# Optimization experiments

Measured on AMD Instinct MI355X. Metric: run time of the kernel, lower is better.

Reference implementation:

```python
import jax, jax.numpy as jnp
import numpy as np

EMBED = 768
HEADS = 12
HEAD_DIM = EMBED // HEADS
STREAMS = 4
SK_ITERS = 20
MLP_HIDDEN = 3072
EPS_SK = 1e-8
EPS_LN = 1e-5


def setup_inputs() -> dict:
    key = jax.random.key(0)
    ks = jax.random.split(key, 16)
    w = lambda k, shape: (jax.random.normal(k, shape, dtype=jnp.float32) * 0.02)
    return {
        "x": jax.random.normal(ks[0], (8, 1024, EMBED), dtype=jnp.float32),
        "ln1_g": jnp.ones((EMBED,), jnp.float32),
        "ln1_b": jnp.zeros((EMBED,), jnp.float32),
        "ln2_g": jnp.ones((EMBED,), jnp.float32),
        "ln2_b": jnp.zeros((EMBED,), jnp.float32),
        "qkv_w": w(ks[1], (3 * EMBED, EMBED)),
        "qkv_b": jnp.zeros((3 * EMBED,), jnp.float32),
        "proj_w": w(ks[2], (EMBED, EMBED)),
        "proj_b": jnp.zeros((EMBED,), jnp.float32),
        "fc1_w": w(ks[3], (MLP_HIDDEN, EMBED)),
        "fc1_b": jnp.zeros((MLP_HIDDEN,), jnp.float32),
        "fc2_w": w(ks[4], (EMBED, MLP_HIDDEN)),
        "fc2_b": jnp.zeros((EMBED,), jnp.float32),
        "a_hres": w(ks[5], (STREAMS, STREAMS)),
        "a_hpre": w(ks[6], (STREAMS,)),
        "a_hpost": w(ks[7], (STREAMS,)),
        "m_hres": w(ks[8], (STREAMS, STREAMS)),
        "m_hpre": w(ks[9], (STREAMS,)),
        "m_hpost": w(ks[10], (STREAMS,)),
    }


def layernorm(x, g, b):
    mu = x.mean(-1, keepdims=True)
    var = ((x - mu) ** 2).mean(-1, keepdims=True)
    return (x - mu) * jax.lax.rsqrt(var + EPS_LN) * g + b


def sinkhorn_knopp(logits):
    # logits: (n, n) -> doubly-stochastic (n, n); batch expansion in torch is redundant
    A = jnp.exp(logits)
    for _ in range(SK_ITERS):
        A = A / (A.sum(-1, keepdims=True) + EPS_SK)
        A = A / (A.sum(-2, keepdims=True) + EPS_SK)
    return A


def attention(x, qkv_w, qkv_b, proj_w, proj_b):
    B, N, D = x.shape
    qkv = x @ qkv_w.T + qkv_b                      # (B, N, 3D)
    qkv = qkv.reshape(B, N, 3, HEADS, HEAD_DIM)
    q, k, v = jnp.moveaxis(qkv, 2, 0)              # each (B, N, H, hd)
    scale = HEAD_DIM ** -0.5
    scores = jnp.einsum('bqhd,bkhd->bhqk', q, k) * scale
    attn = jax.nn.softmax(scores, axis=-1)
    out = jnp.einsum('bhqk,bkhd->bqhd', attn, v).reshape(B, N, D)
    return out @ proj_w.T + proj_b


def mlp(x, fc1_w, fc1_b, fc2_w, fc2_b):
    h = jax.nn.gelu(x @ fc1_w.T + fc1_b, approximate=False)
    return h @ fc2_w.T + fc2_b


def mhc(x, hres_logits, hpre_logits, hpost_logits, transform_fn):
    B, L, D = x.shape
    n, c = STREAMS, D // STREAMS
    xs = x.reshape(B, L, n, c)
    H_res = sinkhorn_knopp(hres_logits)            # (n, n)
    H_pre = jax.nn.softmax(hpre_logits)            # (n,)
    H_post = jax.nn.softmax(hpost_logits)          # (n,)
    x_pre = jnp.einsum('n,blnc->blc', H_pre, xs)   # weighted sum over streams
    x_pre_full = jnp.tile(x_pre, (1, 1, n))        # (B, L, D)
    t = transform_fn(x_pre_full)
    t_mean = t.reshape(B, L, n, c).mean(axis=2)    # (B, L, c)
    out = (jnp.einsum('nm,blmc->blnc', H_res, xs)
           + H_post[None, None, :, None] * t_mean[:, :, None, :])
    return out.reshape(B, L, D)


def reference(x, ln1_g, ln1_b, ln2_g, ln2_b, qkv_w, qkv_b, proj_w, proj_b,
              fc1_w, fc1_b, fc2_w, fc2_b,
              a_hres, a_hpre, a_hpost, m_hres, m_hpre, m_hpost):
    x = mhc(x, a_hres, a_hpre, a_hpost,
            lambda h: attention(layernorm(h, ln1_g, ln1_b), qkv_w, qkv_b, proj_w, proj_b))
    x = mhc(x, m_hres, m_hpre, m_hpost,
            lambda h: mlp(layernorm(h, ln2_g, ln2_b), fc1_w, fc1_b, fc2_w, fc2_b))
    return x
```

## Files before the change

kernel.cpp:

```cpp
#include <hip/hip_runtime.h>
#include <hip/hip_bf16.h>
#include <cstdint>
#include <cstddef>

#define EMBED 768
#define STREAMS 4
#define CHUNK 192
#define HEADS 12
#define HD 64
#define SEQ 1024
#define BATCH 8
#define TOKENS (BATCH * SEQ)
#define MLPH 3072

typedef __bf16 bf16;
typedef __bf16 bf16x4 __attribute__((ext_vector_type(4)));
typedef __bf16 bf16x8 __attribute__((ext_vector_type(8)));
typedef float f32x4 __attribute__((ext_vector_type(4)));

#define GLDS16(gp, lp)                                                        \
  __builtin_amdgcn_global_load_lds(                                           \
      (const __attribute__((address_space(1))) void*)(gp),                    \
      (__attribute__((address_space(3))) void*)(lp), 16, 0, 0)

#define BARRIER() do { asm volatile("" ::: "memory");                         \
  __builtin_amdgcn_s_barrier(); asm volatile("" ::: "memory"); } while (0)

__global__ void hprep_kernel(const float* ar, const float* ap, const float* ao,
                             const float* mr, const float* mp, const float* mo,
                             float* HS) {
  if (threadIdx.x != 0) return;
  const float* L[2] = {ar, mr};
  const float* P[2] = {ap, mp};
  const float* O[2] = {ao, mo};
  for (int s = 0; s < 2; ++s) {
    float A[16];
    for (int i = 0; i < 16; ++i) A[i] = expf(L[s][i]);
    for (int it = 0; it < 20; ++it) {
      for (int r = 0; r < 4; ++r) {
        float rs = A[4*r] + A[4*r+1] + A[4*r+2] + A[4*r+3] + 1e-8f;
        for (int c = 0; c < 4; ++c) A[4*r+c] /= rs;
      }
      for (int c = 0; c < 4; ++c) {
        float cs = A[c] + A[4+c] + A[8+c] + A[12+c] + 1e-8f;
        for (int r = 0; r < 4; ++r) A[4*r+c] /= cs;
      }
    }
    float* dst = HS + s * 24;
    for (int i = 0; i < 16; ++i) dst[i] = A[i];
    {
      float m = fmaxf(fmaxf(P[s][0], P[s][1]), fmaxf(P[s][2], P[s][3]));
      float e[4], t = 0.f;
      for (int i = 0; i < 4; ++i) { e[i] = expf(P[s][i] - m); t += e[i]; }
      for (int i = 0; i < 4; ++i) dst[16 + i] = e[i] / t;
    }
    {
      float m = fmaxf(fmaxf(O[s][0], O[s][1]), fmaxf(O[s][2], O[s][3]));
      float e[4], t = 0.f;
      for (int i = 0; i < 4; ++i) { e[i] = expf(O[s][i] - m); t += e[i]; }
      for (int i = 0; i < 4; ++i) dst[20 + i] = e[i] / t;
    }
  }
}

__global__ void cvt_kernel(const float* __restrict__ in, bf16* __restrict__ out, int n4) {
  int i = blockIdx.x * 256 + threadIdx.x;
  const int st = gridDim.x * 256;
  for (; i < n4; i += st) {
    const float4 v = ((const float4*)in)[i];
    bf16x4 o = {(bf16)v.x, (bf16)v.y, (bf16)v.z, (bf16)v.w};
    *(bf16x4*)(out + (size_t)i * 4) = o;
  }
}

__global__ __launch_bounds__(256) void preln_kernel(
    const float* __restrict__ x, const float* __restrict__ H,
    const float* __restrict__ g, const float* __restrict__ b,
    bf16* __restrict__ out) {
  const int t = blockIdx.x;
  const float* xr = x + (size_t)t * EMBED;
  __shared__ float s[CHUNK];
  __shared__ float part[8];
  __shared__ float red[2];
  const int tid = threadIdx.x;
  float sv = 0.f;
  if (tid < CHUNK) {
    sv = H[0]*xr[tid] + H[1]*xr[CHUNK+tid] + H[2]*xr[2*CHUNK+tid] + H[3]*xr[3*CHUNK+tid];
    s[tid] = sv;
  }
  float sum = sv, sq = sv * sv;
  #pragma unroll
  for (int m = 32; m > 0; m >>= 1) {
    sum += __shfl_down(sum, m);
    sq  += __shfl_down(sq, m);
  }
  if ((tid & 63) == 0) { part[tid >> 6] = sum; part[4 + (tid >> 6)] = sq; }
  __syncthreads();
  if (tid == 0) {
    float S = part[0] + part[1] + part[2] + part[3];
    float Q = part[4] + part[5] + part[6] + part[7];
    float mu = S * (1.f / CHUNK);
    float var = Q * (1.f / CHUNK) - mu * mu;
    red[0] = mu;
    red[1] = rsqrtf(var + 1e-5f);
  }
  __syncthreads();
  const float mu = red[0], rs = red[1];
  bf16* orow = out + (size_t)t * EMBED;
  #pragma unroll
  for (int r = 0; r < 3; ++r) {
    const int d = tid + r * 256;
    const float v = (s[d % CHUNK] - mu) * rs * g[d] + b[d];
    orow[d] = (bf16)v;
  }
}

template <int GELU, int OUTF32>
__global__ __launch_bounds__(256) void gemm_bt(
    const bf16* __restrict__ A, const bf16* __restrict__ B,
    const float* __restrict__ bias, void* __restrict__ Cout,
    int M, int N, int K) {
  constexpr int BM = 128, BN = 128, BK = 32;
  __shared__ bf16 sA[2][BM * BK];
  __shared__ bf16 sB[2][BN * BK];
  const int tid  = threadIdx.x;
  const int lane = tid & 63;
  const int nwg = gridDim.x * gridDim.y;
  int Lw = blockIdx.y * gridDim.x + blockIdx.x;
  Lw = (Lw & 7) * (nwg >> 3) + (Lw >> 3);
  const int bm = (Lw / gridDim.x) * BM;
  const int bn = (Lw % gridDim.x) * BN;
  const int wave = tid >> 6;
  const int wr = (wave >> 1) * 64;
  const int wc = (wave & 1) * 64;
  f32x4 acc[4][4] = {};
  const int tr = tid >> 2;
  const int tc = (tid & 3) * 8;
  const bf16* Ag = A + (size_t)(bm + tr) * K + tc;
  const bf16* Bg = B + (size_t)(bn + tr) * K + tc;
  const int lofs = tr * BK + tc;
  const int arow = wr + (lane & 15);
  const int brow = wc + (lane & 15);
  const int k0 = (lane >> 4) * 8;
  const int nst = K / BK;
  GLDS16(Ag, sA[0] + lofs);
  GLDS16(Ag + (size_t)64 * K, sA[0] + lofs + 64 * BK);
  GLDS16(Bg, sB[0] + lofs);
  GLDS16(Bg + (size_t)64 * K, sB[0] + lofs + 64 * BK);
  for (int t = 0; t < nst; ++t) {
    const int cur = t & 1;
    if (t + 1 < nst) {
      const int bk = (t + 1) * BK;
      GLDS16(Ag + bk, sA[cur ^ 1] + lofs);
      GLDS16(Ag + (size_t)64 * K + bk, sA[cur ^ 1] + lofs + 64 * BK);
      GLDS16(Bg + bk, sB[cur ^ 1] + lofs);
      GLDS16(Bg + (size_t)64 * K + bk, sB[cur ^ 1] + lofs + 64 * BK);
      asm volatile("s_waitcnt vmcnt(4)" ::: "memory");
    } else {
      asm volatile("s_waitcnt vmcnt(0)" ::: "memory");
    }
    BARRIER();
    bf16x8 af[4], bfr[4];
    #pragma unroll
    for (int i = 0; i < 4; ++i) af[i] = *(const bf16x8*)(sA[cur] + (arow + i * 16) * BK + k0);
    #pragma unroll
    for (int j = 0; j < 4; ++j) bfr[j] = *(const bf16x8*)(sB[cur] + (brow + j * 16) * BK + k0);
    #pragma unroll
    for (int i = 0; i < 4; ++i)
      #pragma unroll
      for (int j = 0; j < 4; ++j)
        acc[i][j] = __builtin_amdgcn_mfma_f32_16x16x32_bf16(af[i], bfr[j], acc[i][j], 0, 0, 0);
    BARRIER();
  }
  const int row0 = bm + wr + ((lane >> 4) * 4);
  const int col0 = bn + wc + (lane & 15);
  #pragma unroll
  for (int j = 0; j < 4; ++j) {
    const int col = col0 + j * 16;
    const float bv = bias[col];
    #pragma unroll
    for (int i = 0; i < 4; ++i) {
      #pragma unroll
      for (int r = 0; r < 4; ++r) {
        float v = acc[i][j][r] + bv;
        if (GELU) v = 0.5f * v * (1.f + erff(v * 0.70710678118654752f));
        const size_t off = (size_t)(row0 + i * 16 + r) * N + col;
        if (OUTF32) ((float*)Cout)[off] = v;
        else        ((bf16*)Cout)[off] = (bf16)v;
      }
    }
  }
}

__global__ __launch_bounds__(256) void vt_kernel(const bf16* __restrict__ qkv,
                                                 bf16* __restrict__ VT) {
  const int tt = blockIdx.x;
  const int bh = blockIdx.y;
  const int bb = bh / HEADS;
  const int h = bh - bb * HEADS;
  __shared__ bf16 sT[64 * 64];
  const int t = threadIdx.x;
  const int srow = t >> 3;
  const int g = t & 7;
  const int gs = ((g ^ (srow & 7)) * 8);
  const bf16* Vg = qkv + ((size_t)(bb * SEQ + tt * 64 + srow)) * 2304 + 1536 + h * 64;
  GLDS16(Vg + gs, sT + srow * 64 + g * 8);
  GLDS16(Vg + (size_t)32 * 2304 + gs, sT + (32 + srow) * 64 + g * 8);
  __syncthreads();
  const int hd = t >> 2;
  const int tg = (t & 3) * 16;
  bf16 tmp[16];
  #pragma unroll
  for (int j = 0; j < 16; ++j) {
    const int tok = tg + j;
    tmp[j] = sT[tok * 64 + (hd ^ ((tok & 7) << 3))];
  }
  bf16* op = VT + (size_t)bh * (HD * SEQ) + (size_t)hd * SEQ + tt * 64 + tg;
  *(bf16x8*)(op) = *(const bf16x8*)(tmp);
  *(bf16x8*)(op + 8) = *(const bf16x8*)(tmp + 8);
}

__global__ __launch_bounds__(256) void attn_kernel(
    const bf16* __restrict__ qkv, const bf16* __restrict__ VT,
    bf16* __restrict__ out) {
  const int qt = blockIdx.x;
  const int bh = blockIdx.y;
  const int bb = bh / HEADS;
  const int h = bh - bb * HEADS;
  const int tid = threadIdx.x;
  const int lane = tid & 63;
  const int wave = tid >> 6;
  const size_t tokBase = (size_t)bb * SEQ;
  const int q0 = qt * 64;

  __shared__ bf16 sQ[64 * 64];
  __shared__ bf16 sK[2][64 * 64];
  __shared__ bf16 sV[2][80 * 64];
  __shared__ bf16 sP[4][16 * 64];

  for (int idx = tid; idx < 16 * 64; idx += 256) {
    const bf16 v = (idx < 64) ? (bf16)1.f : (bf16)0.f;
    sV[0][64 * 64 + idx] = v;
    sV[1][64 * 64 + idx] = v;
  }

  const int srow = tid >> 3;
  const int g = tid & 7;
  const int gs = ((g ^ (srow & 7)) * 8);
  {
    const bf16* Qg = qkv + (tokBase + q0 + srow) * 2304 + h * 64;
    GLDS16(Qg + gs, sQ + srow * 64 + g * 8);
    GLDS16(Qg + (size_t)32 * 2304 + gs, sQ + (32 + srow) * 64 + g * 8);
  }
  __syncthreads();
  const int l15 = lane & 15, hi = lane >> 4;
  const int ksw = (l15 & 7) << 3;
  bf16x8 qf[2];
  {
    const int qrow = wave * 16 + l15;
    const int qsw = (qrow & 7) << 3;
    #pragma unroll
    for (int ks = 0; ks < 2; ++ks)
      qf[ks] = *(const bf16x8*)(sQ + qrow * 64 + ((hi * 8 + ks * 32) ^ qsw));
  }

  f32x4 o[5] = {};
  float mrun[4];
  #pragma unroll
  for (int r = 0; r < 4; ++r) mrun[r] = -1e30f;

  const bf16* Kbase = qkv + tokBase * 2304 + 768 + h * 64;
  const bf16* Vbase = VT + (size_t)bh * (HD * SEQ);

  {
    const bf16* Kg = Kbase + (size_t)srow * 2304;
    GLDS16(Kg + gs, sK[0] + srow * 64 + g * 8);
    GLDS16(Kg + (size_t)32 * 2304 + gs, sK[0] + (32 + srow) * 64 + g * 8);
    const bf16* Vg = Vbase + (size_t)srow * SEQ;
    GLDS16(Vg + gs, sV[0] + srow * 64 + g * 8);
    GLDS16(Vg + (size_t)32 * SEQ + gs, sV[0] + (32 + srow) * 64 + g * 8);
  }

  for (int it = 0; it < SEQ / 64; ++it) {
    const int cur = it & 1;
    if (it + 1 < SEQ / 64) {
      const int kb = (it + 1) * 64;
      const bf16* Kg = Kbase + (size_t)(kb + srow) * 2304;
      GLDS16(Kg + gs, sK[cur ^ 1] + srow * 64 + g * 8);
      GLDS16(Kg + (size_t)32 * 2304 + gs, sK[cur ^ 1] + (32 + srow) * 64 + g * 8);
      const bf16* Vg = Vbase + (size_t)srow * SEQ + kb;
      GLDS16(Vg + gs, sV[cur ^ 1] + srow * 64 + g * 8);
      GLDS16(Vg + (size_t)32 * SEQ + gs, sV[cur ^ 1] + (32 + srow) * 64 + g * 8);
      asm volatile("s_waitcnt vmcnt(4)" ::: "memory");
    } else {
      asm volatile("s_waitcnt vmcnt(0)" ::: "memory");
    }
    BARRIER();
    f32x4 s[4];
    #pragma unroll
    for (int nj = 0; nj < 4; ++nj) {
      s[nj] = (f32x4){0.f, 0.f, 0.f, 0.f};
      #pragma unroll
      for (int ks = 0; ks < 2; ++ks) {
        bf16x8 kf = *(const bf16x8*)(sK[cur] + (nj * 16 + l15) * 64 + ((hi * 8 + ks * 32) ^ ksw));
        s[nj] = __builtin_amdgcn_mfma_f32_16x16x32_bf16(qf[ks], kf, s[nj], 0, 0, 0);
      }
    }
    float p[4][4], tmax[4];
    #pragma unroll
    for (int r = 0; r < 4; ++r) {
      float m = fmaxf(fmaxf(s[0][r], s[1][r]), fmaxf(s[2][r], s[3][r]));
      tmax[r] = m * 0.125f;
    }
    #pragma unroll
    for (int r = 0; r < 4; ++r) {
      #pragma unroll
      for (int mm = 1; mm < 16; mm <<= 1) tmax[r] = fmaxf(tmax[r], __shfl_xor(tmax[r], mm));
    }
    float alpha[4];
    #pragma unroll
    for (int r = 0; r < 4; ++r) {
      const float mnew = fmaxf(mrun[r], tmax[r]);
      alpha[r] = __expf(mrun[r] - mnew);
      mrun[r] = mnew;
      #pragma unroll
      for (int nj = 0; nj < 4; ++nj)
        p[nj][r] = __expf(s[nj][r] * 0.125f - mnew);
    }
    #pragma unroll
    for (int nj = 0; nj < 5; ++nj)
      #pragma unroll
      for (int r = 0; r < 4; ++r)
        o[nj][r] *= alpha[r];
    bf16* Pw = sP[wave];
    #pragma unroll
    for (int r = 0; r < 4; ++r) {
      const int prow = hi * 4 + r;
      const int psw = (prow & 7) << 3;
      #pragma unroll
      for (int nj = 0; nj < 4; ++nj)
        Pw[prow * 64 + ((nj * 16 + l15) ^ psw)] = (bf16)p[nj][r];
    }
    #pragma unroll
    for (int ks = 0; ks < 2; ++ks) {
      bf16x8 pa = *(const bf16x8*)(Pw + l15 * 64 + ((hi * 8 + ks * 32) ^ ksw));
      #pragma unroll
      for (int nj = 0; nj < 5; ++nj) {
        bf16x8 vb = *(const bf16x8*)(sV[cur] + (nj * 16 + l15) * 64 + ((hi * 8 + ks * 32) ^ ksw));
        o[nj] = __builtin_amdgcn_mfma_f32_16x16x32_bf16(pa, vb, o[nj], 0, 0, 0);
      }
    }
    BARRIER();
  }
  #pragma unroll
  for (int r = 0; r < 4; ++r) {
    const float lsum = __shfl(o[4][r], hi << 4, 64);
    const float inv = 1.f / lsum;
    const size_t row = tokBase + q0 + wave * 16 + hi * 4 + r;
    bf16* orow = out + row * EMBED + h * 64;
    #pragma unroll
    for (int nj = 0; nj < 4; ++nj)
      orow[nj * 16 + l15] = (bf16)(o[nj][r] * inv);
  }
}

__global__ void combine_kernel(const float* __restrict__ xs, const float* __restrict__ t,
                               const float* __restrict__ Hres, const float* __restrict__ Hpost,
                               float* __restrict__ outp) {
  const int idx = blockIdx.x * 256 + threadIdx.x;
  if (idx >= TOKENS * CHUNK) return;
  const int tok = idx / CHUNK;
  const int c = idx - tok * CHUNK;
  const float* xr = xs + (size_t)tok * EMBED + c;
  const float* tr = t + (size_t)tok * EMBED + c;
  const float x0 = xr[0], x1 = xr[CHUNK], x2 = xr[2 * CHUNK], x3 = xr[3 * CHUNK];
  const float tm = 0.25f * (tr[0] + tr[CHUNK] + tr[2 * CHUNK] + tr[3 * CHUNK]);
  #pragma unroll
  for (int n = 0; n < 4; ++n) {
    const float v = Hres[4*n+0]*x0 + Hres[4*n+1]*x1 + Hres[4*n+2]*x2 + Hres[4*n+3]*x3
                  + Hpost[n] * tm;
    outp[(size_t)tok * EMBED + n * CHUNK + c] = v;
  }
}

extern "C" void kernel_launch(void* const* d_in, const int* in_sizes, int n_in,
                              void* d_out, int out_size, void* d_ws, size_t ws_size,
                              hipStream_t stream) {
  const float* x       = (const float*)d_in[0];
  const float* ln1_g   = (const float*)d_in[1];
  const float* ln1_b   = (const float*)d_in[2];
  const float* ln2_g   = (const float*)d_in[3];
  const float* ln2_b   = (const float*)d_in[4];
  const float* qkv_w   = (const float*)d_in[5];
  const float* qkv_b   = (const float*)d_in[6];
  const float* proj_w  = (const float*)d_in[7];
  const float* proj_b  = (const float*)d_in[8];
  const float* fc1_w   = (const float*)d_in[9];
  const float* fc1_b   = (const float*)d_in[10];
  const float* fc2_w   = (const float*)d_in[11];
  const float* fc2_b   = (const float*)d_in[12];
  const float* a_hres  = (const float*)d_in[13];
  const float* a_hpre  = (const float*)d_in[14];
  const float* a_hpost = (const float*)d_in[15];
  const float* m_hres  = (const float*)d_in[16];
  const float* m_hpre  = (const float*)d_in[17];
  const float* m_hpost = (const float*)d_in[18];

  char* ws = (char*)d_ws;
  float* HS = (float*)(ws);
  bf16* Wq  = (bf16*)(ws + 1024);
  bf16* Wp  = (bf16*)(ws + 1024 + 3538944);
  bf16* W1  = (bf16*)(ws + 1024 + 3538944 + 1179648);
  bf16* W2  = (bf16*)(ws + 1024 + 3538944 + 1179648 + 4718592);
  bf16* LN  = (bf16*)(ws + 14156800);
  float* T  = (float*)(ws + 26739712);
  float* X2 = (float*)(ws + 51905536);
  bf16* QKV = (bf16*)(ws + 77071360);
  bf16* AO  = (bf16*)(ws + 114820096);
  bf16* Hm  = (bf16*)(ws + 77071360);
  bf16* VT  = LN;

  hprep_kernel<<<1, 64, 0, stream>>>(a_hres, a_hpre, a_hpost, m_hres, m_hpre, m_hpost, HS);
  cvt_kernel<<<1024, 256, 0, stream>>>(qkv_w, Wq, 2304 * 768 / 4);
  cvt_kernel<<<1024, 256, 0, stream>>>(proj_w, Wp, 768 * 768 / 4);
  cvt_kernel<<<1024, 256, 0, stream>>>(fc1_w, W1, 3072 * 768 / 4);
  cvt_kernel<<<1024, 256, 0, stream>>>(fc2_w, W2, 768 * 3072 / 4);

  preln_kernel<<<TOKENS, 256, 0, stream>>>(x, HS + 16, ln1_g, ln1_b, LN);
  gemm_bt<0, 0><<<dim3(2304 / 128, TOKENS / 128), 256, 0, stream>>>(LN, Wq, qkv_b, QKV, TOKENS, 2304, 768);
  vt_kernel<<<dim3(16, 96), 256, 0, stream>>>(QKV, VT);
  attn_kernel<<<dim3(16, 96), 256, 0, stream>>>(QKV, VT, AO);
  gemm_bt<0, 1><<<dim3(768 / 128, TOKENS / 128), 256, 0, stream>>>(AO, Wp, proj_b, T, TOKENS, 768, 768);
  combine_kernel<<<(TOKENS * CHUNK + 255) / 256, 256, 0, stream>>>(x, T, HS + 0, HS + 20, X2);

  preln_kernel<<<TOKENS, 256, 0, stream>>>(X2, HS + 24 + 16, ln2_g, ln2_b, LN);
  gemm_bt<1, 0><<<dim3(3072 / 128, TOKENS / 128), 256, 0, stream>>>(LN, W1, fc1_b, Hm, TOKENS, 3072, 768);
  gemm_bt<0, 1><<<dim3(768 / 128, TOKENS / 128), 256, 0, stream>>>(Hm, W2, fc2_b, T, TOKENS, 768, 3072);
  combine_kernel<<<(TOKENS * CHUNK + 255) / 256, 256, 0, stream>>>(X2, T, HS + 24, HS + 24 + 20, (float*)d_out);
}
```

Baseline: 369.0 us.

## Use 32x32 MFMA with triple buffering in GEMM; remap and lazily rescale attention

The GEMM kernel moves from 16x16x32 to 32x32x16 MFMA tiles, adds an XOR swizzle on its LDS layout, and goes from double to triple buffering with a two-stage-ahead prefetch. The attention kernel switches to a 1D grid remapped so that groups of eight heads share a query tile, and it skips the online-softmax rescale when no row maximum grows. These aim to cut LDS fragment loads and bank conflicts, hide more global latency, and drop exp and multiply work. The costs are more LDS per block, which may lower occupancy, and a wave-uniform branch in the attention inner loop.

```diff
diff --git a/kernel.cpp b/kernel.cpp
--- a/kernel.cpp
+++ b/kernel.cpp
@@ -17,6 +17,7 @@
 typedef __bf16 bf16x4 __attribute__((ext_vector_type(4)));
 typedef __bf16 bf16x8 __attribute__((ext_vector_type(8)));
 typedef float f32x4 __attribute__((ext_vector_type(4)));
+typedef float f32x16 __attribute__((ext_vector_type(16)));
 
 #define GLDS16(gp, lp)                                                        \
   __builtin_amdgcn_global_load_lds(                                           \
@@ -121,8 +122,8 @@
     const float* __restrict__ bias, void* __restrict__ Cout,
     int M, int N, int K) {
   constexpr int BM = 128, BN = 128, BK = 32;
-  __shared__ bf16 sA[2][BM * BK];
-  __shared__ bf16 sB[2][BN * BK];
+  __shared__ bf16 sA[3][BM * BK];
+  __shared__ bf16 sB[3][BN * BK];
   const int tid  = threadIdx.x;
   const int lane = tid & 63;
   const int nwg = gridDim.x * gridDim.y;
@@ -133,58 +134,70 @@
   const int wave = tid >> 6;
   const int wr = (wave >> 1) * 64;
   const int wc = (wave & 1) * 64;
-  f32x4 acc[4][4] = {};
+  f32x16 acc[2][2] = {};
   const int tr = tid >> 2;
-  const int tc = (tid & 3) * 8;
-  const bf16* Ag = A + (size_t)(bm + tr) * K + tc;
-  const bf16* Bg = B + (size_t)(bn + tr) * K + tc;
-  const int lofs = tr * BK + tc;
-  const int arow = wr + (lane & 15);
-  const int brow = wc + (lane & 15);
-  const int k0 = (lane >> 4) * 8;
+  const int gt = tid & 3;
+  const int gsw = (gt ^ (tr & 3)) * 8;
+  const bf16* Ag = A + (size_t)(bm + tr) * K + gsw;
+  const bf16* Bg = B + (size_t)(bn + tr) * K + gsw;
+  const int lofs = tr * BK + gt * 8;
+  const int r31 = lane & 31, rh = lane >> 5;
+  const int asw = r31 & 3;
   const int nst = K / BK;
-  GLDS16(Ag, sA[0] + lofs);
-  GLDS16(Ag + (size_t)64 * K, sA[0] + lofs + 64 * BK);
-  GLDS16(Bg, sB[0] + lofs);
-  GLDS16(Bg + (size_t)64 * K, sB[0] + lofs + 64 * BK);
+#define STAGE(buf, t)                                                         \
+  do { const int bk_ = (t) * BK;                                              \
+    GLDS16(Ag + bk_, sA[buf] + lofs);                                         \
+    GLDS16(Ag + (size_t)64 * K + bk_, sA[buf] + lofs + 64 * BK);              \
+    GLDS16(Bg + bk_, sB[buf] + lofs);                                         \
+    GLDS16(Bg + (size_t)64 * K + bk_, sB[buf] + lofs + 64 * BK);              \
+  } while (0)
+  STAGE(0, 0);
+  STAGE(1, 1);
+  int cur = 0;
   for (int t = 0; t < nst; ++t) {
-    const int cur = t & 1;
-    if (t + 1 < nst) {
-      const int bk = (t + 1) * BK;
-      GLDS16(Ag + bk, sA[cur ^ 1] + lofs);
-      GLDS16(Ag + (size_t)64 * K + bk, sA[cur ^ 1] + lofs + 64 * BK);
-      GLDS16(Bg + bk, sB[cur ^ 1] + lofs);
-      GLDS16(Bg + (size_t)64 * K + bk, sB[cur ^ 1] + lofs + 64 * BK);
+    if (t + 2 < nst) {
+      const int nb = cur + 2 >= 3 ? cur - 1 : cur + 2;
+      STAGE(nb, t + 2);
+      asm volatile("s_waitcnt vmcnt(8)" ::: "memory");
+    } else if (t + 1 < nst) {
       asm volatile("s_waitcnt vmcnt(4)" ::: "memory");
     } else {
       asm volatile("s_waitcnt vmcnt(0)" ::: "memory");
     }
     BARRIER();
-    bf16x8 af[4], bfr[4];
-    #pragma unroll
-    for (int i = 0; i < 4; ++i) af[i] = *(const bf16x8*)(sA[cur] + (arow + i * 16) * BK + k0);
-    #pragma unroll
-    for (int j = 0; j < 4; ++j) bfr[j] = *(const bf16x8*)(sB[cur] + (brow + j * 16) * BK + k0);
-    #pragma unroll
-    for (int i = 0; i < 4; ++i)
-      #pragma unroll
-      for (int j = 0; j < 4; ++j)
-        acc[i][j] = __builtin_amdgcn_mfma_f32_16x16x32_bf16(af[i], bfr[j], acc[i][j], 0, 0, 0);
+    bf16x8 af[2][2], bfr[2][2];
+    #pragma unroll
+    for (int i = 0; i < 2; ++i)
+      #pragma unroll
+      for (int ks = 0; ks < 2; ++ks) {
+        const int pos = ((ks * 2 + rh) ^ asw) * 8;
+        af[i][ks]  = *(const bf16x8*)(sA[cur] + (wr + i * 32 + r31) * BK + pos);
+        bfr[i][ks] = *(const bf16x8*)(sB[cur] + (wc + i * 32 + r31) * BK + pos);
+      }
+    #pragma unroll
+    for (int ks = 0; ks < 2; ++ks)
+      #pragma unroll
+      for (int i = 0; i < 2; ++i)
+        #pragma unroll
+        for (int j = 0; j < 2; ++j)
+          acc[i][j] = __builtin_amdgcn_mfma_f32_32x32x16_bf16(af[i][ks], bfr[j][ks], acc[i][j], 0, 0, 0);
     BARRIER();
-  }
-  const int row0 = bm + wr + ((lane >> 4) * 4);
-  const int col0 = bn + wc + (lane & 15);
-  #pragma unroll
-  for (int j = 0; j < 4; ++j) {
-    const int col = col0 + j * 16;
+    cur = cur == 2 ? 0 : cur + 1;
+  }
+#undef STAGE
+  #pragma unroll
+  for (int j = 0; j < 2; ++j) {
+    const int col = bn + wc + j * 32 + r31;
     const float bv = bias[col];
     #pragma unroll
-    for (int i = 0; i < 4; ++i) {
-      #pragma unroll
-      for (int r = 0; r < 4; ++r) {
-        float v = acc[i][j][r] + bv;
+    for (int i = 0; i < 2; ++i) {
+      const int row0 = bm + wr + i * 32 + 4 * rh;
+      #pragma unroll
+      for (int reg = 0; reg < 16; ++reg) {
+        const int row = row0 + (reg & 3) + 8 * (reg >> 2);
+        float v = acc[i][j][reg] + bv;
         if (GELU) v = 0.5f * v * (1.f + erff(v * 0.70710678118654752f));
-        const size_t off = (size_t)(row0 + i * 16 + r) * N + col;
+        const size_t off = (size_t)row * N + col;
         if (OUTF32) ((float*)Cout)[off] = v;
         else        ((bf16*)Cout)[off] = (bf16)v;
       }
@@ -223,8 +236,9 @@
 __global__ __launch_bounds__(256) void attn_kernel(
     const bf16* __restrict__ qkv, const bf16* __restrict__ VT,
     bf16* __restrict__ out) {
-  const int qt = blockIdx.x;
-  const int bh = blockIdx.y;
+  const int lin = blockIdx.x;
+  const int qt = (lin >> 3) & 15;
+  const int bh = (lin & 7) + 8 * (lin >> 7);
   const int bb = bh / HEADS;
   const int h = bh - bb * HEADS;
   const int tid = threadIdx.x;
@@ -306,7 +320,7 @@
         s[nj] = __builtin_amdgcn_mfma_f32_16x16x32_bf16(qf[ks], kf, s[nj], 0, 0, 0);
       }
     }
-    float p[4][4], tmax[4];
+    float tmax[4];
     #pragma unroll
     for (int r = 0; r < 4; ++r) {
       float m = fmaxf(fmaxf(s[0][r], s[1][r]), fmaxf(s[2][r], s[3][r]));
@@ -317,21 +331,29 @@
       #pragma unroll
       for (int mm = 1; mm < 16; mm <<= 1) tmax[r] = fmaxf(tmax[r], __shfl_xor(tmax[r], mm));
     }
-    float alpha[4];
-    #pragma unroll
-    for (int r = 0; r < 4; ++r) {
-      const float mnew = fmaxf(mrun[r], tmax[r]);
-      alpha[r] = __expf(mrun[r] - mnew);
-      mrun[r] = mnew;
+    bool need = false;
+    #pragma unroll
+    for (int r = 0; r < 4; ++r) need |= (tmax[r] > mrun[r]);
+    if (__any(need)) {
+      float alpha[4];
+      #pragma unroll
+      for (int r = 0; r < 4; ++r) {
+        const float mnew = fmaxf(mrun[r], tmax[r]);
+        alpha[r] = __expf(mrun[r] - mnew);
+        mrun[r] = mnew;
+      }
+      #pragma unroll
+      for (int nj = 0; nj < 5; ++nj)
+        #pragma unroll
+        for (int r = 0; r < 4; ++r)
+          o[nj][r] *= alpha[r];
+    }
+    float p[4][4];
+    #pragma unroll
+    for (int r = 0; r < 4; ++r)
       #pragma unroll
       for (int nj = 0; nj < 4; ++nj)
-        p[nj][r] = __expf(s[nj][r] * 0.125f - mnew);
-    }
-    #pragma unroll
-    for (int nj = 0; nj < 5; ++nj)
-      #pragma unroll
-      for (int r = 0; r < 4; ++r)
-        o[nj][r] *= alpha[r];
+        p[nj][r] = __expf(s[nj][r] * 0.125f - mrun[r]);
     bf16* Pw = sP[wave];
     #pragma unroll
     for (int r = 0; r < 4; ++r) {
@@ -429,7 +451,7 @@
   preln_kernel<<<TOKENS, 256, 0, stream>>>(x, HS + 16, ln1_g, ln1_b, LN);
   gemm_bt<0, 0><<<dim3(2304 / 128, TOKENS / 128), 256, 0, stream>>>(LN, Wq, qkv_b, QKV, TOKENS, 2304, 768);
   vt_kernel<<<dim3(16, 96), 256, 0, stream>>>(QKV, VT);
-  attn_kernel<<<dim3(16, 96), 256, 0, stream>>>(QKV, VT, AO);
+  attn_kernel<<<1536, 256, 0, stream>>>(QKV, VT, AO);
   gemm_bt<0, 1><<<dim3(768 / 128, TOKENS / 128), 256, 0, stream>>>(AO, Wp, proj_b, T, TOKENS, 768, 768);
   combine_kernel<<<(TOKENS * CHUNK + 255) / 256, 256, 0, stream>>>(x, T, HS + 0, HS + 20, X2);
 
```

Result: slower. 390.7 us (+5.9%).
